# Optimization experiments

Hardware: AMD Instinct MI355X
Metric: run time of the kernel (lower is better)

## Reference

```python
import jax, jax.numpy as jnp
import numpy as np

EPS = 1e-5
K = 9
DILATION = 1

def bn(x, g, b, m, v):
    # x: (B,C,N,1), inference-mode BatchNorm2d with running stats
    sh = (1, -1, 1, 1)
    return (x - m.reshape(sh)) * (g.reshape(sh) / jnp.sqrt(v.reshape(sh) + EPS)) + b.reshape(sh)

def conv1x1(x, w, b):
    # w: (Cout, Cin), x: (B,Cin,N,1)
    return jnp.einsum('oc,bcnj->bonj', w, x) + b.reshape(1, -1, 1, 1)

def knn_idx(feat, k):
    # feat: (B,C,N) -> (B,N,k) indices of k nearest nodes (incl. self)
    xt = jnp.transpose(feat, (0, 2, 1))  # (B,N,C)
    x2 = jnp.sum(xt * xt, axis=-1)       # (B,N)
    dist = x2[:, :, None] - 2.0 * jnp.einsum('bnc,bmc->bnm', xt, xt) + x2[:, None, :]
    _, idx = jax.lax.top_k(-dist, k)
    return idx

def setup_inputs():
    key = jax.random.key(0)
    ks = jax.random.split(key, 24)
    B, C, H, W = 16, 256, 32, 32
    HID = 512
    def g(i, shape, s=1.0):
        return jax.random.normal(ks[i], shape, dtype=jnp.float32) * s
    def pos(i, shape):
        return jax.random.uniform(ks[i], shape, dtype=jnp.float32, minval=0.5, maxval=1.5)
    return {
        'x': g(0, (B, C, H, W)),
        'fc1_w': g(1, (C, C), 0.05), 'fc1_b': g(2, (C,), 0.05),
        'bn1_g': pos(3, (C,)), 'bn1_b': g(4, (C,), 0.1), 'bn1_m': g(5, (C,), 0.1), 'bn1_v': pos(6, (C,)),
        'gc_w': g(7, (HID, 2 * C), 0.05), 'gc_b': g(8, (HID,), 0.05),
        'gbn_g': pos(9, (HID,)), 'gbn_b': g(10, (HID,), 0.1), 'gbn_m': g(11, (HID,), 0.1), 'gbn_v': pos(12, (HID,)),
        'bn2_g': pos(13, (HID,)), 'bn2_b': g(14, (HID,), 0.1), 'bn2_m': g(15, (HID,), 0.1), 'bn2_v': pos(16, (HID,)),
        'fc2_w': g(17, (C, HID), 0.05), 'fc2_b': g(18, (C,), 0.05),
        'bn3_g': pos(19, (C,)), 'bn3_b': g(20, (C,), 0.1), 'bn3_m': g(21, (C,), 0.1), 'bn3_v': pos(22, (C,)),
    }

def reference(x, fc1_w, fc1_b, bn1_g, bn1_b, bn1_m, bn1_v,
              gc_w, gc_b, gbn_g, gbn_b, gbn_m, gbn_v,
              bn2_g, bn2_b, bn2_m, bn2_v,
              fc2_w, fc2_b, bn3_g, bn3_b, bn3_m, bn3_v):
    B, C, H, W = x.shape
    N = H * W
    x = x.reshape(B, C, N, 1)
    shortcut = x
    # fc1: 1x1 conv + BN
    h = bn(conv1x1(x, fc1_w, fc1_b), bn1_g, bn1_b, bn1_m, bn1_v)
    # DyGraphConv2d: dynamic dilated kNN graph over N nodes
    feat = h[..., 0]  # (B,C,N)
    idx = knn_idx(feat, K * DILATION)[:, :, ::DILATION]  # (B,N,K)
    # MRConv2d: max over neighbors of (x_j - x_i)
    x_j = jax.vmap(lambda f, i: f[:, i])(feat, idx)        # (B,C,N,K) gather
    diff_max = jnp.max(x_j - feat[:, :, :, None], axis=-1)  # (B,C,N)
    # interleave [x, max_diff] along channel dim -> (B, 2C, N, 1)
    m = jnp.stack([feat, diff_max], axis=2).reshape(B, 2 * C, N, 1)
    g = conv1x1(m, gc_w, gc_b)
    g = bn(g, gbn_g, gbn_b, gbn_m, gbn_v)  # BasicConv BN, act='None'
    # graph_conv Sequential: BN + GELU (erf, torch default)
    g = jax.nn.gelu(bn(g, bn2_g, bn2_b, bn2_m, bn2_v), approximate=False)
    # fc2 + residual (drop_path=0 -> identity)
    out = bn(conv1x1(g, fc2_w, fc2_b), bn3_g, bn3_b, bn3_m, bn3_v)
    return out + shortcut
```

## Files before the change

### kernel.cpp

```cpp
#include <hip/hip_runtime.h>
#include <hip/hip_bf16.h>
#include <stdint.h>

typedef unsigned long long u64;
typedef __hip_bfloat16 bf16;
typedef short s8v __attribute__((ext_vector_type(8)));
typedef short s4v __attribute__((ext_vector_type(4)));
typedef float f4v __attribute__((ext_vector_type(4)));

#define B_   16
#define C_   256
#define N_   1024
#define HID_ 512

#define GLD16(g, l)                                                         \
    __builtin_amdgcn_global_load_lds(                                       \
        (const __attribute__((address_space(1))) void*)(g),                 \
        (__attribute__((address_space(3))) void*)(l), 16, 0, 0)

#define WAITB4() do {                                                       \
        asm volatile("s_waitcnt vmcnt(4)" ::: "memory");                    \
        __builtin_amdgcn_s_barrier();                                       \
        __builtin_amdgcn_sched_barrier(0);                                  \
    } while (0)
#define WAITB2() do {                                                       \
        asm volatile("s_waitcnt vmcnt(2)" ::: "memory");                    \
        __builtin_amdgcn_s_barrier();                                       \
        __builtin_amdgcn_sched_barrier(0);                                  \
    } while (0)
#define WAITB0() do {                                                       \
        asm volatile("s_waitcnt vmcnt(0)" ::: "memory");                    \
        __builtin_amdgcn_s_barrier();                                       \
        __builtin_amdgcn_sched_barrier(0);                                  \
    } while (0)

__device__ __forceinline__ unsigned short f2b(float f) {
    unsigned u = __float_as_uint(f);
    unsigned r = (u + 0x7FFFu + ((u >> 16) & 1u)) >> 16;
    return (unsigned short)r;
}
__device__ __forceinline__ float b2f(unsigned short s) {
    return __uint_as_float(((unsigned)s) << 16);
}
__device__ __forceinline__ float ldIn(const void* p, long long i, int bf) {
    return bf ? b2f(((const unsigned short*)p)[i]) : ((const float*)p)[i];
}
__device__ __forceinline__ u64 shfl_xor_u64(u64 v, int m) {
    unsigned lo = (unsigned)v, hi = (unsigned)(v >> 32);
    lo = __shfl_xor(lo, m, 64);
    hi = __shfl_xor(hi, m, 64);
    return ((u64)hi << 32) | lo;
}

__global__ __launch_bounds__(256)
void cast_prep(const void* xp, const void* w1, const void* wg, const void* w2,
    const void* fc1_b, const void* bn1_g, const void* bn1_b, const void* bn1_m, const void* bn1_v,
    const void* gc_b,  const void* gbn_g, const void* gbn_b, const void* gbn_m, const void* gbn_v,
    const void* bn2_g, const void* bn2_b, const void* bn2_m, const void* bn2_v,
    const void* fc2_b, const void* bn3_g, const void* bn3_b, const void* bn3_m, const void* bn3_v,
    short* W1h, short* W1l, short* Wgb, short* W2b,
    int* flags, float* s1, float* t1, float* Sg, float* Tg, float* s3, float* t3,
    float* x2)
{
    __shared__ int sf;
    int t = threadIdx.x;
    if (t == 0) {
        const unsigned short* u = (const unsigned short*)xp;
        int cnt = 0;
        for (int i = 0; i < 64; ++i) {
            int e = (u[2 * i] >> 7) & 0xFF;
            cnt += (e >= 87 && e <= 167);
        }
        sf = (cnt >= 48) ? 1 : 0;
    }
    __syncthreads();
    int inf = sf;
    int bid = blockIdx.x;

    if (bid == 1792) {
        if (t == 0) flags[0] = inf;
        int i = t;
        {
            float g = ldIn(bn1_g, i, inf), bb = ldIn(bn1_b, i, inf);
            float m = ldIn(bn1_m, i, inf), v  = ldIn(bn1_v, i, inf);
            float s = g / sqrtf(v + 1e-5f);
            s1[i] = s;
            t1[i] = (ldIn(fc1_b, i, inf) - m) * s + bb;

            float g3 = ldIn(bn3_g, i, inf), b3 = ldIn(bn3_b, i, inf);
            float m3 = ldIn(bn3_m, i, inf), v3 = ldIn(bn3_v, i, inf);
            float ss3 = g3 / sqrtf(v3 + 1e-5f);
            s3[i] = ss3;
            t3[i] = (ldIn(fc2_b, i, inf) - m3) * ss3 + b3;
        }
        #pragma unroll
        for (int pass = 0; pass < 2; ++pass) {
            int j = t + pass * 256;
            float gg = ldIn(gbn_g, j, inf), gb = ldIn(gbn_b, j, inf);
            float gm = ldIn(gbn_m, j, inf), gv = ldIn(gbn_v, j, inf);
            float sg = gg / sqrtf(gv + 1e-5f);
            float g2 = ldIn(bn2_g, j, inf), b2 = ldIn(bn2_b, j, inf);
            float m2 = ldIn(bn2_m, j, inf), v2 = ldIn(bn2_v, j, inf);
            float s2 = g2 / sqrtf(v2 + 1e-5f);
            Sg[j] = sg * s2;
            Tg[j] = ((ldIn(gc_b, j, inf) - gm) * sg + gb - m2) * s2 + b2;
        }
        return;
    }

    if (bid < 64) x2[bid * 256 + t] = 0.f;

    long long i = (long long)bid * 256 + t;
    if (i < 65536) {
        float f = ldIn(w1, i, inf);
        unsigned short h = f2b(f);
        W1h[i] = (short)h;
        W1l[i] = (short)f2b(f - b2f(h));
    } else if (i < 65536 + 262144) {
        long long j = i - 65536;
        Wgb[j] = (short)f2b(ldIn(wg, j, inf));
    } else {
        long long j = i - 327680;
        W2b[j] = (short)f2b(ldIn(w2, j, inf));
    }
}

__global__ __launch_bounds__(256)
void transpose_split_x(const void* __restrict__ X, short* __restrict__ xth,
                       short* __restrict__ xtl, const int* __restrict__ flags)
{
    __shared__ float tile[64][68];
    int inf = flags[0];
    int t = threadIdx.x;
    int n0 = blockIdx.x * 64, c0 = blockIdx.y * 64, b = blockIdx.z;

    #pragma unroll
    for (int rr = 0; rr < 4; ++rr) {
        int cl = (t >> 4) + rr * 16;
        int nl = (t & 15) * 4;
        long long g = ((long long)b * C_ + c0 + cl) * N_ + n0 + nl;
        if (inf) {
            s4v v = *(const s4v*)((const short*)X + g);
            tile[cl][nl + 0] = b2f((unsigned short)v[0]);
            tile[cl][nl + 1] = b2f((unsigned short)v[1]);
            tile[cl][nl + 2] = b2f((unsigned short)v[2]);
            tile[cl][nl + 3] = b2f((unsigned short)v[3]);
        } else {
            f4v v = *(const f4v*)((const float*)X + g);
            tile[cl][nl + 0] = v[0]; tile[cl][nl + 1] = v[1];
            tile[cl][nl + 2] = v[2]; tile[cl][nl + 3] = v[3];
        }
    }
    __syncthreads();

    int nl = t >> 2, cseg = t & 3;
    long long base = ((long long)((b << 10) + n0 + nl)) * C_ + c0 + cseg * 16;
    s8v h0, h1, l0, l1;
    #pragma unroll
    for (int cc = 0; cc < 16; ++cc) {
        float f = tile[cseg * 16 + cc][nl];
        unsigned short h = f2b(f);
        unsigned short l = f2b(f - b2f(h));
        if (cc < 8) { h0[cc] = (short)h; l0[cc] = (short)l; }
        else        { h1[cc - 8] = (short)h; l1[cc - 8] = (short)l; }
    }
    *(s8v*)(xth + base)     = h0;
    *(s8v*)(xth + base + 8) = h1;
    *(s8v*)(xtl + base)     = l0;
    *(s8v*)(xtl + base + 8) = l1;
}

__global__ __launch_bounds__(256)
void fc1_mfma(const short* __restrict__ W1h, const short* __restrict__ W1l,
              const short* __restrict__ xth, const short* __restrict__ xtl,
              const float* __restrict__ s1, const float* __restrict__ t1,
              float* __restrict__ Ft, short* __restrict__ Fhi,
              short* __restrict__ Flo, float* __restrict__ x2)
{
    __shared__ __align__(16) char ldsbuf[49152];

    int t = threadIdx.x;
    int n0 = blockIdx.x * 64, o0 = blockIdx.y * 128, b = blockIdx.z;
    int wv = t >> 6, lane = t & 63, ln15 = t & 15, quad = (t >> 4) & 3;

    int csw = (((lane & 3) ^ ((lane >> 3) & 3))) * 8;
    const short* gAh = W1h + (long long)(o0 + wv * 32 + (lane >> 2)) * C_ + csw;
    const short* gAl = W1l + (long long)(o0 + wv * 32 + (lane >> 2)) * C_ + csw;
    int slotofs = wv * 32 * 32;

#define FC1_STAGE(kc_) do {                                                   \
        short* base_ = (short*)(ldsbuf + ((kc_) % 3) * 16384);                \
        short* dh = base_ + slotofs;                                          \
        short* dl = base_ + 4096 + slotofs;                                   \
        GLD16(gAh + (kc_) * 32,            dh);                               \
        GLD16(gAh + (kc_) * 32 + 16 * C_,  dh + 16 * 32);                     \
        GLD16(gAl + (kc_) * 32,            dl);                               \
        GLD16(gAl + (kc_) * 32 + 16 * C_,  dl + 16 * 32);                     \
    } while (0)

    FC1_STAGE(0);

    s8v xh[8], xl[8];
    {
        long long xoff = (long long)((b << 10) + n0 + wv * 16 + ln15) * C_ + quad * 8;
        #pragma unroll
        for (int kc = 0; kc < 8; ++kc) {
            xh[kc] = *(const s8v*)(xth + xoff + kc * 32);
            xl[kc] = *(const s8v*)(xtl + xoff + kc * 32);
        }
    }

    FC1_STAGE(1);

    f4v acc[8];
    #pragma unroll
    for (int i = 0; i < 8; ++i) acc[i] = 0.f;

    int roff = (quad ^ ((ln15 >> 1) & 3)) * 8;

    #pragma unroll
    for (int kc = 0; kc < 8; ++kc) {
        if (kc < 7) WAITB4(); else WAITB0();
        if (kc < 6) FC1_STAGE(kc + 2);
        const short* Ah_c = (const short*)(ldsbuf + (kc % 3) * 16384);
        const short* Al_c = Ah_c + 4096;
        #pragma unroll
        for (int i = 0; i < 8; ++i) {
            s8v wh8 = *(const s8v*)&Ah_c[(i * 16 + ln15) * 32 + roff];
            s8v wl8 = *(const s8v*)&Al_c[(i * 16 + ln15) * 32 + roff];
            acc[i] = __builtin_amdgcn_mfma_f32_16x16x32_bf16(wh8, xh[kc], acc[i], 0, 0, 0);
            acc[i] = __builtin_amdgcn_mfma_f32_16x16x32_bf16(wh8, xl[kc], acc[i], 0, 0, 0);
            acc[i] = __builtin_amdgcn_mfma_f32_16x16x32_bf16(wl8, xh[kc], acc[i], 0, 0, 0);
        }
    }
#undef FC1_STAGE

    int n = n0 + wv * 16 + ln15;
    long long nb = (long long)(b << 10) + n;
    float p2 = 0.f;
    #pragma unroll
    for (int i = 0; i < 8; ++i) {
        int ob = o0 + i * 16 + quad * 4;
        f4v f;
        s4v hi, lo;
        #pragma unroll
        for (int r = 0; r < 4; ++r) {
            float v = acc[i][r] * s1[ob + r] + t1[ob + r];
            f[r] = v;
            unsigned short h = f2b(v);
            hi[r] = (short)h;
            lo[r] = (short)f2b(v - b2f(h));
            p2 += v * v;
        }
        *(f4v*)(Ft  + nb * C_ + ob) = f;
        *(s4v*)(Fhi + nb * C_ + ob) = hi;
        *(s4v*)(Flo + nb * C_ + ob) = lo;
    }
    p2 += __shfl_xor(p2, 16, 64);
    p2 += __shfl_xor(p2, 32, 64);
    if (quad == 0) atomicAdd(&x2[nb], p2);
}

__global__ __launch_bounds__(256)
void gram_topk(const short* __restrict__ Fhi, const short* __restrict__ Flo,
               const float* __restrict__ x2, u64* __restrict__ Part)
{
    __shared__ __align__(16) char ldsbuf[33280];
    float* x2s = (float*)(ldsbuf + 32768);
    u64*   mrg  = (u64*)(ldsbuf);
    u64*   mrg2 = (u64*)(ldsbuf + 20480);

    int t = threadIdx.x;
    int q0 = blockIdx.x * 64, mq = blockIdx.y, b = blockIdx.z;
    int wv = t >> 6, lane = t & 63, ln15 = t & 15, quad = (t >> 4) & 3;

    int csw = (((lane & 3) ^ ((lane >> 3) & 3))) * 8;
    const short* gAh = Fhi + (long long)((b << 10) + mq * 128 + wv * 32 + (lane >> 2)) * C_ + csw;
    const short* gAl = Flo + (long long)((b << 10) + mq * 128 + wv * 32 + (lane >> 2)) * C_ + csw;
    short* lH0 = (short*)(ldsbuf)           + wv * 32 * 32;
    short* lL0 = (short*)(ldsbuf + 8192)    + wv * 32 * 32;
    short* lH1 = (short*)(ldsbuf + 16384)   + wv * 32 * 32;
    short* lL1 = (short*)(ldsbuf + 24576)   + wv * 32 * 32;

#define GRAM_STAGE(kc_, bi_) do {                                             \
        short* dh = (bi_) ? lH1 : lH0;                                        \
        short* dl = (bi_) ? lL1 : lL0;                                        \
        GLD16(gAh + (kc_) * 32,            dh);                               \
        GLD16(gAh + (kc_) * 32 + 16 * C_,  dh + 16 * 32);                     \
        GLD16(gAl + (kc_) * 32,            dl);                               \
        GLD16(gAl + (kc_) * 32 + 16 * C_,  dl + 16 * 32);                     \
    } while (0)

    GRAM_STAGE(0, 0);

    if (t < 128) x2s[t] = x2[(b << 10) + mq * 128 + t];

    s8v qh[8], ql[8];
    {
        long long qoff = (long long)((b << 10) + q0 + wv * 16 + ln15) * C_ + quad * 8;
        #pragma unroll
        for (int kc = 0; kc < 8; ++kc) {
            qh[kc] = *(const s8v*)(Fhi + qoff + kc * 32);
            ql[kc] = *(const s8v*)(Flo + qoff + kc * 32);
        }
    }

    f4v acc[8];
    #pragma unroll
    for (int i = 0; i < 8; ++i) acc[i] = 0.f;

    int roff = (quad ^ ((ln15 >> 1) & 3)) * 8;

    __syncthreads();

    #pragma unroll
    for (int kc = 0; kc < 8; ++kc) {
        if (kc < 7) GRAM_STAGE(kc + 1, (kc + 1) & 1);
        const short* Ah_c = (const short*)(ldsbuf + (kc & 1) * 16384);
        const short* Al_c = Ah_c + 4096;
        #pragma unroll
        for (int i = 0; i < 8; ++i) {
            s8v mh = *(const s8v*)&Ah_c[(i * 16 + ln15) * 32 + roff];
            s8v ml = *(const s8v*)&Al_c[(i * 16 + ln15) * 32 + roff];
            acc[i] = __builtin_amdgcn_mfma_f32_16x16x32_bf16(mh, qh[kc], acc[i], 0, 0, 0);
            acc[i] = __builtin_amdgcn_mfma_f32_16x16x32_bf16(mh, ql[kc], acc[i], 0, 0, 0);
            acc[i] = __builtin_amdgcn_mfma_f32_16x16x32_bf16(ml, qh[kc], acc[i], 0, 0, 0);
        }
        __syncthreads();
    }
#undef GRAM_STAGE

    u64 l[9];
    #pragma unroll
    for (int i = 0; i < 9; ++i) l[i] = ~0ULL;
    #pragma unroll
    for (int i = 0; i < 8; ++i) {
        #pragma unroll
        for (int r = 0; r < 4; ++r) {
            int mloc = i * 16 + quad * 4 + r;
            float d = x2s[mloc] - 2.f * acc[i][r];
            unsigned u = __float_as_uint(d);
            u = (u & 0x80000000u) ? ~u : (u | 0x80000000u);
            u64 key = ((u64)u << 32) | (unsigned)(mq * 128 + mloc);
            if (key < l[8]) {
                u64 x = key;
                #pragma unroll
                for (int jj = 0; jj < 9; ++jj) {
                    u64 lo2 = l[jj] < x ? l[jj] : x;
                    u64 hi2 = l[jj] < x ? x : l[jj];
                    l[jj] = lo2; x = hi2;
                }
            }
        }
    }

    __syncthreads();
    {
        int qloc = wv * 16 + ln15;
        #pragma unroll
        for (int k = 0; k < 9; ++k) mrg[(qloc * 4 + quad) * 9 + k] = l[k];
    }
    __syncthreads();
    if (t < 128) {
        int r = t >> 1, pr = t & 1;
        const u64* LA = &mrg[(r * 4 + pr * 2) * 9];
        const u64* LB = LA + 9;
        int ia = 0, ib = 0;
        u64* Po = &mrg2[(r * 2 + pr) * 9];
        #pragma unroll
        for (int k = 0; k < 9; ++k) {
            u64 va = LA[ia], vb = LB[ib];
            bool ta = va < vb;
            Po[k] = ta ? va : vb;
            ia += ta; ib += !ta;
        }
    }
    __syncthreads();
    if (t < 64) {
        const u64* LA = &mrg2[(t * 2) * 9];
        const u64* LB = LA + 9;
        int ia = 0, ib = 0;
        u64* P = Part + (((long long)((b << 10) + q0 + t)) * 8 + mq) * 9;
        #pragma unroll
        for (int k = 0; k < 9; ++k) {
            u64 va = LA[ia], vb = LB[ib];
            bool ta = va < vb;
            P[k] = ta ? va : vb;
            ia += ta; ib += !ta;
        }
    }
}

__global__ __launch_bounds__(256)
void build_Mt(const float* __restrict__ Ft, const u64* __restrict__ Part,
              short* __restrict__ Mt)
{
    int t = threadIdx.x;
    int wv = t >> 6, lane = t & 63;
    int n = blockIdx.x * 4 + wv;
    int b = blockIdx.y;
    long long nb = (long long)(b << 10) + n;

    const u64* L = Part + nb * 72 + (long long)(lane & 7) * 9;
    u64 l[9];
    #pragma unroll
    for (int k = 0; k < 9; ++k) l[k] = L[k];
    #pragma unroll
    for (int s = 1; s <= 4; s <<= 1) {
        u64 p[9];
        #pragma unroll
        for (int k = 0; k < 9; ++k) p[k] = shfl_xor_u64(l[k], s);
        #pragma unroll
        for (int k = 0; k < 9; ++k) {
            u64 x = p[k];
            if (x < l[8]) {
                #pragma unroll
                for (int jj = 0; jj < 9; ++jj) {
                    u64 lo2 = l[jj] < x ? l[jj] : x;
                    u64 hi2 = l[jj] < x ? x : l[jj];
                    l[jj] = lo2; x = hi2;
                }
            }
        }
    }

    int c0 = lane * 4;
    f4v f = *(const f4v*)(Ft + nb * C_ + c0);
    f4v mx = {-3.4e38f, -3.4e38f, -3.4e38f, -3.4e38f};
    #pragma unroll
    for (int k = 0; k < 9; ++k) {
        int id = (int)(l[k] & 0xFFFFFFFFu);
        f4v g = *(const f4v*)(Ft + ((long long)(b << 10) + id) * C_ + c0);
        mx[0] = fmaxf(mx[0], g[0]); mx[1] = fmaxf(mx[1], g[1]);
        mx[2] = fmaxf(mx[2], g[2]); mx[3] = fmaxf(mx[3], g[3]);
    }
    s8v m8;
    #pragma unroll
    for (int r = 0; r < 4; ++r) {
        m8[2 * r]     = (short)f2b(f[r]);
        m8[2 * r + 1] = (short)f2b(mx[r] - f[r]);
    }
    *(s8v*)(Mt + nb * (2 * C_) + 2 * c0) = m8;
}

template<int EPI, int K_>
__global__ __launch_bounds__(256)
void mfma_gemm(const short* __restrict__ A, const short* __restrict__ Bm,
               void* __restrict__ Out, const float* __restrict__ scale,
               const float* __restrict__ bias, const void* __restrict__ resid,
               const int* __restrict__ flags, int Odim)
{
    __shared__ __align__(16) char ldsbuf[32768];

    int t = threadIdx.x, b = blockIdx.z;
    int n0 = blockIdx.x * 64, o0 = blockIdx.y * 128;
    int wv = t >> 6, lane = t & 63, ln15 = t & 15, quad = (t >> 4) & 3;

    int csw = (((lane & 3) ^ ((lane >> 3) & 3))) * 8;
    const short* gA = A + (long long)(o0 + wv * 32 + (lane >> 2)) * K_ + csw;
    int slotofs = wv * 32 * 32;

#define GEMM_STAGE(kc_) do {                                                  \
        short* d = (short*)(ldsbuf + ((kc_) & 3) * 8192) + slotofs;           \
        GLD16(gA + (kc_) * 32,            d);                                 \
        GLD16(gA + (kc_) * 32 + 16 * K_,  d + 16 * 32);                       \
    } while (0)

    GEMM_STAGE(0);

    constexpr int NKC = K_ / 32;
    s8v bfr[NKC];
    {
        long long boff = (long long)((b << 10) + n0 + wv * 16 + ln15) * K_ + quad * 8;
        #pragma unroll
        for (int kc = 0; kc < NKC; ++kc)
            bfr[kc] = *(const s8v*)(Bm + boff + kc * 32);
    }

    GEMM_STAGE(1);
    GEMM_STAGE(2);

    f4v acc[8];
    #pragma unroll
    for (int i = 0; i < 8; ++i) acc[i] = 0.f;

    int roff = (quad ^ ((ln15 >> 1) & 3)) * 8;

    #pragma unroll
    for (int kc = 0; kc < NKC; ++kc) {
        if (kc < NKC - 2) WAITB4();
        else if (kc == NKC - 2) WAITB2();
        else WAITB0();
        if (kc < NKC - 3) GEMM_STAGE(kc + 3);
        const short* Ac = (const short*)(ldsbuf + (kc & 3) * 8192);
        #pragma unroll
        for (int i = 0; i < 8; ++i) {
            s8v a = *(const s8v*)&Ac[(i * 16 + ln15) * 32 + roff];
            acc[i] = __builtin_amdgcn_mfma_f32_16x16x32_bf16(a, bfr[kc], acc[i], 0, 0, 0);
        }
    }
#undef GEMM_STAGE

    int inf = flags[0];
    int n = n0 + wv * 16 + ln15;
    #pragma unroll
    for (int i = 0; i < 8; ++i) {
        int ob = o0 + i * 16 + quad * 4;
        if (EPI == 0) {
            s4v g;
            #pragma unroll
            for (int r = 0; r < 4; ++r) {
                float val = acc[i][r] * scale[ob + r] + bias[ob + r];
                val = 0.5f * val * (1.0f + erff(val * 0.70710678118654752f));
                g[r] = (short)f2b(val);
            }
            *(s4v*)((short*)Out + ((long long)((b << 10) + n)) * Odim + ob) = g;
        } else {
            #pragma unroll
            for (int r = 0; r < 4; ++r) {
                int o = ob + r;
                long long oi = ((long long)b * Odim + o) * N_ + n;
                ((float*)Out)[oi] = acc[i][r] * scale[o] + bias[o] + ldIn(resid, oi, inf);
            }
        }
    }
}

extern "C" void kernel_launch(void* const* d_in, const int* in_sizes, int n_in,
                              void* d_out, int out_size, void* d_ws, size_t ws_size,
                              hipStream_t stream)
{
    const void* p[23];
    if (n_in >= 23 && in_sizes[0] != 4194304 && in_sizes[22] == 4194304) {
        const int amap[23] = {
            22, 13, 12, 1, 0, 2, 3,
            21, 20, 17, 16, 18, 19,
            5, 4, 6, 7,
            15, 14, 9, 8, 10, 11 };
        for (int i = 0; i < 23; ++i) p[i] = d_in[amap[i]];
    } else {
        for (int i = 0; i < 23; ++i) p[i] = d_in[i];
    }

    const void* x     = p[0];
    const void* fc1_w = p[1];
    const void* fc1_b = p[2];
    const void* bn1_g = p[3];
    const void* bn1_b = p[4];
    const void* bn1_m = p[5];
    const void* bn1_v = p[6];
    const void* gc_w  = p[7];
    const void* gc_b  = p[8];
    const void* gbn_g = p[9];
    const void* gbn_b = p[10];
    const void* gbn_m = p[11];
    const void* gbn_v = p[12];
    const void* bn2_g = p[13];
    const void* bn2_b = p[14];
    const void* bn2_m = p[15];
    const void* bn2_v = p[16];
    const void* fc2_w = p[17];
    const void* fc2_b = p[18];
    const void* bn3_g = p[19];
    const void* bn3_b = p[20];
    const void* bn3_m = p[21];
    const void* bn3_v = p[22];

    char* ws = (char*)d_ws;
    size_t off = 0;
    int*   flags = (int*)ws;
    float* s1 = (float*)(ws + 256);
    float* t1 = s1 + 256;
    float* s3 = t1 + 256;
    float* t3 = s3 + 256;
    float* Sg = t3 + 256;
    float* Tg = Sg + 512;
    off = 16384;
    short* W1h   = (short*)(ws + off); off += (size_t)C_ * C_ * 2;
    short* W1l   = (short*)(ws + off); off += (size_t)C_ * C_ * 2;
    short* Wgb   = (short*)(ws + off); off += (size_t)HID_ * 2 * C_ * 2;
    short* W2b   = (short*)(ws + off); off += (size_t)C_ * HID_ * 2;
    short* xth   = (short*)(ws + off); off += (size_t)B_ * N_ * C_ * 2;
    short* xtl   = (short*)(ws + off); off += (size_t)B_ * N_ * C_ * 2;
    float* Ft    = (float*)(ws + off); off += (size_t)B_ * N_ * C_ * 4;
    short* Fhi   = (short*)(ws + off); off += (size_t)B_ * N_ * C_ * 2;
    short* Flo   = (short*)(ws + off); off += (size_t)B_ * N_ * C_ * 2;
    float* x2    = (float*)(ws + off); off += (size_t)B_ * N_ * 4;
    u64*   Part  = (u64*)  (ws + off); off += (size_t)B_ * N_ * 8 * 9 * 8;
    short* Mt    = (short*)(ws + off); off += (size_t)B_ * N_ * 2 * C_ * 2;
    short* Gt    = (short*)(ws + off); off += (size_t)B_ * N_ * HID_ * 2;

    cast_prep<<<1793, 256, 0, stream>>>(x, fc1_w, gc_w, fc2_w,
        fc1_b, bn1_g, bn1_b, bn1_m, bn1_v,
        gc_b, gbn_g, gbn_b, gbn_m, gbn_v,
        bn2_g, bn2_b, bn2_m, bn2_v,
        fc2_b, bn3_g, bn3_b, bn3_m, bn3_v,
        W1h, W1l, Wgb, W2b,
        flags, s1, t1, Sg, Tg, s3, t3, x2);

    transpose_split_x<<<dim3(16, 4, 16), 256, 0, stream>>>(x, xth, xtl, flags);

    fc1_mfma<<<dim3(16, 2, 16), 256, 0, stream>>>(
        W1h, W1l, xth, xtl, s1, t1, Ft, Fhi, Flo, x2);

    gram_topk<<<dim3(16, 8, 16), 256, 0, stream>>>(Fhi, Flo, x2, Part);

    build_Mt<<<dim3(256, 16), 256, 0, stream>>>(Ft, Part, Mt);

    mfma_gemm<0, 512><<<dim3(16, 4, 16), 256, 0, stream>>>(
        Wgb, Mt, Gt, Sg, Tg, nullptr, flags, HID_);

    mfma_gemm<1, 512><<<dim3(16, 2, 16), 256, 0, stream>>>(
        W2b, Gt, d_out, s3, t3, x, flags, C_);
}
```

Measured before the change: 280.0 us.

## Shrink fc1 output tile, double-buffer with syncthreads, compute row norms separately

Measured after the change: 296.4 us. 5.9% more time.

```diff
diff --git a/kernel.cpp b/kernel.cpp
--- a/kernel.cpp
+++ b/kernel.cpp
@@ -175,30 +175,30 @@
               const short* __restrict__ xth, const short* __restrict__ xtl,
               const float* __restrict__ s1, const float* __restrict__ t1,
               float* __restrict__ Ft, short* __restrict__ Fhi,
-              short* __restrict__ Flo, float* __restrict__ x2)
-{
-    __shared__ __align__(16) char ldsbuf[49152];
+              short* __restrict__ Flo)
+{
+    __shared__ __align__(16) char ldsbuf[32768];
 
     int t = threadIdx.x;
-    int n0 = blockIdx.x * 64, o0 = blockIdx.y * 128, b = blockIdx.z;
+    int n0 = blockIdx.x * 64, o0 = blockIdx.y * 64, b = blockIdx.z;
     int wv = t >> 6, lane = t & 63, ln15 = t & 15, quad = (t >> 4) & 3;
 
     int csw = (((lane & 3) ^ ((lane >> 3) & 3))) * 8;
-    const short* gAh = W1h + (long long)(o0 + wv * 32 + (lane >> 2)) * C_ + csw;
-    const short* gAl = W1l + (long long)(o0 + wv * 32 + (lane >> 2)) * C_ + csw;
-    int slotofs = wv * 32 * 32;
-
-#define FC1_STAGE(kc_) do {                                                   \
-        short* base_ = (short*)(ldsbuf + ((kc_) % 3) * 16384);                \
-        short* dh = base_ + slotofs;                                          \
-        short* dl = base_ + 4096 + slotofs;                                   \
-        GLD16(gAh + (kc_) * 32,            dh);                               \
-        GLD16(gAh + (kc_) * 32 + 16 * C_,  dh + 16 * 32);                     \
-        GLD16(gAl + (kc_) * 32,            dl);                               \
-        GLD16(gAl + (kc_) * 32 + 16 * C_,  dl + 16 * 32);                     \
+    const short* gAh = W1h + (long long)(o0 + wv * 16 + (lane >> 2)) * C_ + csw;
+    const short* gAl = W1l + (long long)(o0 + wv * 16 + (lane >> 2)) * C_ + csw;
+    short* lH0 = (short*)(ldsbuf)           + wv * 16 * 32;
+    short* lL0 = (short*)(ldsbuf + 8192)    + wv * 16 * 32;
+    short* lH1 = (short*)(ldsbuf + 16384)   + wv * 16 * 32;
+    short* lL1 = (short*)(ldsbuf + 24576)   + wv * 16 * 32;
+
+#define FC1_STAGE(kc_, bi_) do {                                              \
+        short* dh = (bi_) ? lH1 : lH0;                                        \
+        short* dl = (bi_) ? lL1 : lL0;                                        \
+        GLD16(gAh + (kc_) * 32, dh);                                          \
+        GLD16(gAl + (kc_) * 32, dl);                                          \
     } while (0)
 
-    FC1_STAGE(0);
+    FC1_STAGE(0, 0);
 
     s8v xh[8], xl[8];
     {
@@ -210,36 +210,35 @@
         }
     }
 
-    FC1_STAGE(1);
-
-    f4v acc[8];
-    #pragma unroll
-    for (int i = 0; i < 8; ++i) acc[i] = 0.f;
+    f4v acc[4];
+    #pragma unroll
+    for (int i = 0; i < 4; ++i) acc[i] = 0.f;
 
     int roff = (quad ^ ((ln15 >> 1) & 3)) * 8;
 
+    __syncthreads();
+
     #pragma unroll
     for (int kc = 0; kc < 8; ++kc) {
-        if (kc < 7) WAITB4(); else WAITB0();
-        if (kc < 6) FC1_STAGE(kc + 2);
-        const short* Ah_c = (const short*)(ldsbuf + (kc % 3) * 16384);
+        if (kc < 7) FC1_STAGE(kc + 1, (kc + 1) & 1);
+        const short* Ah_c = (const short*)(ldsbuf + (kc & 1) * 16384);
         const short* Al_c = Ah_c + 4096;
         #pragma unroll
-        for (int i = 0; i < 8; ++i) {
+        for (int i = 0; i < 4; ++i) {
             s8v wh8 = *(const s8v*)&Ah_c[(i * 16 + ln15) * 32 + roff];
             s8v wl8 = *(const s8v*)&Al_c[(i * 16 + ln15) * 32 + roff];
             acc[i] = __builtin_amdgcn_mfma_f32_16x16x32_bf16(wh8, xh[kc], acc[i], 0, 0, 0);
             acc[i] = __builtin_amdgcn_mfma_f32_16x16x32_bf16(wh8, xl[kc], acc[i], 0, 0, 0);
             acc[i] = __builtin_amdgcn_mfma_f32_16x16x32_bf16(wl8, xh[kc], acc[i], 0, 0, 0);
         }
+        __syncthreads();
     }
 #undef FC1_STAGE
 
     int n = n0 + wv * 16 + ln15;
     long long nb = (long long)(b << 10) + n;
-    float p2 = 0.f;
-    #pragma unroll
-    for (int i = 0; i < 8; ++i) {
+    #pragma unroll
+    for (int i = 0; i < 4; ++i) {
         int ob = o0 + i * 16 + quad * 4;
         f4v f;
         s4v hi, lo;
@@ -250,15 +249,38 @@
             unsigned short h = f2b(v);
             hi[r] = (short)h;
             lo[r] = (short)f2b(v - b2f(h));
-            p2 += v * v;
         }
         *(f4v*)(Ft  + nb * C_ + ob) = f;
         *(s4v*)(Fhi + nb * C_ + ob) = hi;
         *(s4v*)(Flo + nb * C_ + ob) = lo;
     }
-    p2 += __shfl_xor(p2, 16, 64);
-    p2 += __shfl_xor(p2, 32, 64);
-    if (quad == 0) atomicAdd(&x2[nb], p2);
+}
+
+__global__ __launch_bounds__(256)
+void calc_x2(const float* __restrict__ Ft, float* __restrict__ x2)
+{
+    long long nb = (long long)blockIdx.x * 256 + threadIdx.x;
+    const float* row = Ft + nb * C_;
+    float tot = 0.f;
+    #pragma unroll
+    for (int half = 0; half < 2; ++half) {
+        float p[4];
+        #pragma unroll
+        for (int q = 0; q < 4; ++q) {
+            float s = 0.f;
+            #pragma unroll
+            for (int i = 0; i < 8; ++i) {
+                f4v v = *(const f4v*)(row + half * 128 + i * 16 + q * 4);
+                s += v[0] * v[0];
+                s += v[1] * v[1];
+                s += v[2] * v[2];
+                s += v[3] * v[3];
+            }
+            p[q] = s;
+        }
+        tot += (p[0] + p[1]) + (p[2] + p[3]);
+    }
+    x2[nb] = tot;
 }
 
 __global__ __launch_bounds__(256)
@@ -600,8 +622,10 @@
 
     transpose_split_x<<<dim3(16, 4, 16), 256, 0, stream>>>(x, xth, xtl, flags);
 
-    fc1_mfma<<<dim3(16, 2, 16), 256, 0, stream>>>(
-        W1h, W1l, xth, xtl, s1, t1, Ft, Fhi, Flo, x2);
+    fc1_mfma<<<dim3(16, 4, 16), 256, 0, stream>>>(
+        W1h, W1l, xth, xtl, s1, t1, Ft, Fhi, Flo);
+
+    calc_x2<<<64, 256, 0, stream>>>(Ft, x2);
 
     gram_topk<<<dim3(16, 8, 16), 256, 0, stream>>>(Fhi, Flo, x2, Part);
 
```
